# Kernel tuning notes

Measured on AMD Instinct MI355X. Metric: run time of the kernel, lower is better.

Reference implementation:

```python
import jax, jax.numpy as jnp
import numpy as np

Q_MAX = 127.0  # int8 symmetric quantization range

def _ste_round(v):
    # straight-through round (matches quantize-forward semantics)
    return v + jax.lax.stop_gradient(jnp.round(v) - v)

def setup_inputs() -> dict:
    key = jax.random.key(0)
    k1, k2, k3, k4 = jax.random.split(key, 4)
    B, S, D_IN, D_OUT = 32, 577, 1024, 2560
    x = jax.random.normal(k1, (B, S, D_IN), dtype=jnp.float32)
    # pre-quantized int8 weight stored as int32 for jax friendliness
    w_int = jax.random.randint(k2, (D_OUT, D_IN), -127, 128, dtype=jnp.int32)
    # per-output-row dequant scales (absmax/127 style, small positive)
    scale_w = jax.random.uniform(k3, (D_OUT,), dtype=jnp.float32, minval=0.005, maxval=0.02)
    bias = jax.random.normal(k4, (D_OUT,), dtype=jnp.float32)
    return {"x": x, "w_int": w_int, "scale_w": scale_w, "bias": bias}

def reference(x, w_int, scale_w, bias):
    # bnb Int8Linear: dynamic per-row int8 quantization of activations,
    # per-column (output-feature) weight scales, then bias add.
    # x: [B, S, D_in], w_int: [D_out, D_in] in [-127,127], scale_w: [D_out]
    absmax_x = jnp.max(jnp.abs(x), axis=-1, keepdims=True)  # [B, S, 1]
    scale_x = jnp.maximum(absmax_x, 1e-8) / Q_MAX
    x_q = _ste_round(x / scale_x)  # quantized activations in [-127, 127]
    # integer-valued GEMM carried in fp32 accumulation
    acc = jnp.einsum("bsd,od->bso", x_q, w_int.astype(jnp.float32))
    y = acc * scale_x * scale_w[None, None, :] + bias[None, None, :]
    return y
```

## Files before the change

### kernel.cpp

```cpp
#include <hip/hip_runtime.h>
#include <stdint.h>

typedef int v4i __attribute__((ext_vector_type(4)));

__device__ __forceinline__ void gll16(const void* g, void* l) {
    __builtin_amdgcn_global_load_lds(
        (const __attribute__((address_space(1))) void*)(uintptr_t)g,
        (__attribute__((address_space(3))) void*)(uint32_t)(uintptr_t)l,
        16, 0, 0);
}

__global__ __launch_bounds__(256) void quant_x(const float* __restrict__ x,
                                               signed char* __restrict__ xq,
                                               float* __restrict__ sx, int M) {
    const int row = blockIdx.x;
    const int tid = threadIdx.x;
    signed char* qrow = xq + (size_t)row * 1024;
    if (row >= M) {
        ((char4*)qrow)[tid] = make_char4(0, 0, 0, 0);
        if (tid == 0) sx[row] = 0.0f;
        return;
    }
    const float4 v = ((const float4*)(x + (size_t)row * 1024))[tid];
    float a = fmaxf(fmaxf(fabsf(v.x), fabsf(v.y)), fmaxf(fabsf(v.z), fabsf(v.w)));
#pragma unroll
    for (int off = 32; off > 0; off >>= 1)
        a = fmaxf(a, __shfl_xor(a, off));
    __shared__ float red[4];
    if ((tid & 63) == 0) red[tid >> 6] = a;
    __syncthreads();
    const float am = fmaxf(fmaxf(red[0], red[1]), fmaxf(red[2], red[3]));
    const float amc = fmaxf(am, 1e-8f);
    const float scale = amc * (1.0f / 127.0f);
    const float inv = 127.0f / amc;
    char4 q;
    q.x = (signed char)(int)rintf(v.x * inv);
    q.y = (signed char)(int)rintf(v.y * inv);
    q.z = (signed char)(int)rintf(v.z * inv);
    q.w = (signed char)(int)rintf(v.w * inv);
    ((char4*)qrow)[tid] = q;
    if (tid == 0) sx[row] = scale;
}

__global__ __launch_bounds__(256) void conv_w(const int* __restrict__ w,
                                              signed char* __restrict__ w8, int n4) {
    const int i = blockIdx.x * 256 + threadIdx.x;
    if (i < n4) {
        const int4 v = ((const int4*)w)[i];
        char4 c;
        c.x = (signed char)v.x; c.y = (signed char)v.y;
        c.z = (signed char)v.z; c.w = (signed char)v.w;
        ((char4*)w8)[i] = c;
    }
}

__global__ __launch_bounds__(256) void gemm_i8(const signed char* __restrict__ xq,
                                               const signed char* __restrict__ w8,
                                               const float* __restrict__ sx,
                                               const float* __restrict__ sw,
                                               const float* __restrict__ bias,
                                               float* __restrict__ out,
                                               int M, int N, int K) {
    __shared__ signed char As[128 * 64];
    __shared__ signed char Bs[128 * 64];

    const int tid  = threadIdx.x;
    const int lane = tid & 63;
    const int wave = tid >> 6;
    const int wm = (wave & 1) * 64;
    const int wn = (wave >> 1) * 64;
    const int m_block = blockIdx.y * 128;
    const int n_block = blockIdx.x * 128;

    v4i acc[4][4];
#pragma unroll
    for (int mt = 0; mt < 4; ++mt)
#pragma unroll
        for (int nt = 0; nt < 4; ++nt) {
            acc[mt][nt].x = 0; acc[mt][nt].y = 0; acc[mt][nt].z = 0; acc[mt][nt].w = 0;
        }

    const int sr = tid >> 2;
    const int sc = ((tid & 3) ^ ((sr >> 1) & 3)) * 16;
    const signed char* aG = xq + (size_t)(m_block + sr) * K + sc;
    const signed char* bG = w8 + (size_t)(n_block + sr) * K + sc;
    signed char* aL = As + wave * 1024;
    signed char* bL = Bs + wave * 1024;

    const int fr  = lane & 15;
    const int fcs = (((lane >> 4) ^ ((lane >> 1) & 3))) * 16;

    for (int k0 = 0; k0 < K; k0 += 64) {
        if (k0) __syncthreads();
        gll16(aG + k0, aL);
        gll16(aG + k0 + (size_t)64 * K, aL + 4096);
        gll16(bG + k0, bL);
        gll16(bG + k0 + (size_t)64 * K, bL + 4096);
        __syncthreads();

        v4i af[4], bf[4];
#pragma unroll
        for (int mt = 0; mt < 4; ++mt)
            af[mt] = *(const v4i*)&As[(wm + mt * 16 + fr) * 64 + fcs];
#pragma unroll
        for (int nt = 0; nt < 4; ++nt)
            bf[nt] = *(const v4i*)&Bs[(wn + nt * 16 + fr) * 64 + fcs];
#pragma unroll
        for (int mt = 0; mt < 4; ++mt)
#pragma unroll
            for (int nt = 0; nt < 4; ++nt)
                acc[mt][nt] = __builtin_amdgcn_mfma_i32_16x16x64_i8(af[mt], bf[nt], acc[mt][nt], 0, 0, 0);
    }

    const int lr = lane >> 4;
    const int lc = lane & 15;
#pragma unroll
    for (int mt = 0; mt < 4; ++mt) {
        const int rbase = m_block + wm + mt * 16 + lr * 4;
        float sxv[4];
#pragma unroll
        for (int r = 0; r < 4; ++r)
            sxv[r] = (rbase + r < M) ? sx[rbase + r] : 0.0f;
#pragma unroll
        for (int nt = 0; nt < 4; ++nt) {
            const int col = n_block + wn + nt * 16 + lc;
            const float swv = sw[col];
            const float bv  = bias[col];
            const int* a = (const int*)&acc[mt][nt];
#pragma unroll
            for (int r = 0; r < 4; ++r) {
                const int row = rbase + r;
                if (row < M)
                    out[(size_t)row * N + col] = (float)a[r] * sxv[r] * swv + bv;
            }
        }
    }
}

extern "C" void kernel_launch(void* const* d_in, const int* in_sizes, int n_in,
                              void* d_out, int out_size, void* d_ws, size_t ws_size,
                              hipStream_t stream) {
    const float* x       = (const float*)d_in[0];
    const int*   w_int   = (const int*)d_in[1];
    const float* scale_w = (const float*)d_in[2];
    const float* bias    = (const float*)d_in[3];
    float* out = (float*)d_out;

    const int D_OUT = in_sizes[2];
    const int D_IN  = in_sizes[1] / D_OUT;
    const int M     = in_sizes[0] / D_IN;
    const int Mpad  = ((M + 127) / 128) * 128;

    signed char* xq = (signed char*)d_ws;
    signed char* w8 = xq + (size_t)Mpad * D_IN;
    float*       sx = (float*)(w8 + (size_t)D_OUT * D_IN);

    quant_x<<<Mpad, 256, 0, stream>>>(x, xq, sx, M);
    const int n4 = D_OUT * D_IN / 4;
    conv_w<<<(n4 + 255) / 256, 256, 0, stream>>>(w_int, w8, n4);
    dim3 grid(D_OUT / 128, Mpad / 128);
    gemm_i8<<<grid, dim3(256, 1, 1), 0, stream>>>(xq, w8, sx, scale_w, bias, out, M, D_OUT, D_IN);
}
```

Before: 317.4 us.

## Enlarge GEMM tile to 256x256 with 8 waves and double-buffered LDS pipeline

The int8 GEMM moves from 128x128 tiles with 4 waves to 256x256 tiles with 8 waves, each wave computing 128x64. Shared memory is double-buffered with global-to-LDS prefetch two K-tiles ahead, manual vmcnt waits, and MFMA work split in two halves around the next stage issue, with raised wave priority during the MFMA sections. The goal is to hide global load latency and raise arithmetic intensity per LDS byte. The costs are more registers and LDS per block, fewer blocks in the grid, and more M padding.

Measured after the change: 324.5 us. 2.2% more time.

```diff
diff --git a/kernel.cpp b/kernel.cpp
--- a/kernel.cpp
+++ b/kernel.cpp
@@ -54,76 +54,104 @@
     }
 }
 
-__global__ __launch_bounds__(256) void gemm_i8(const signed char* __restrict__ xq,
-                                               const signed char* __restrict__ w8,
-                                               const float* __restrict__ sx,
-                                               const float* __restrict__ sw,
-                                               const float* __restrict__ bias,
-                                               float* __restrict__ out,
-                                               int M, int N, int K) {
-    __shared__ signed char As[128 * 64];
-    __shared__ signed char Bs[128 * 64];
+__global__ __launch_bounds__(512, 2) void gemm_i8(const signed char* __restrict__ xq,
+                                                  const signed char* __restrict__ w8,
+                                                  const float* __restrict__ sx,
+                                                  const float* __restrict__ sw,
+                                                  const float* __restrict__ bias,
+                                                  float* __restrict__ out,
+                                                  int M, int N, int K) {
+    __shared__ signed char As[2][16384];
+    __shared__ signed char Bs[2][16384];
 
     const int tid  = threadIdx.x;
     const int lane = tid & 63;
     const int wave = tid >> 6;
-    const int wm = (wave & 1) * 64;
-    const int wn = (wave >> 1) * 64;
-    const int m_block = blockIdx.y * 128;
-    const int n_block = blockIdx.x * 128;
+    const int m_off = (wave >> 2) * 128;
+    const int n_off = (wave & 3) * 64;
+    const int m_block = blockIdx.y * 256;
+    const int n_block = blockIdx.x * 256;
+    const int nt_tiles = K >> 6;
 
-    v4i acc[4][4];
+    v4i acc[8][4];
 #pragma unroll
-    for (int mt = 0; mt < 4; ++mt)
+    for (int mt = 0; mt < 8; ++mt)
 #pragma unroll
         for (int nt = 0; nt < 4; ++nt) {
             acc[mt][nt].x = 0; acc[mt][nt].y = 0; acc[mt][nt].z = 0; acc[mt][nt].w = 0;
         }
 
-    const int sr = tid >> 2;
-    const int sc = ((tid & 3) ^ ((sr >> 1) & 3)) * 16;
-    const signed char* aG = xq + (size_t)(m_block + sr) * K + sc;
-    const signed char* bG = w8 + (size_t)(n_block + sr) * K + sc;
-    signed char* aL = As + wave * 1024;
-    signed char* bL = Bs + wave * 1024;
+    const int sc = ((tid & 3) ^ ((tid >> 3) & 3)) * 16;
+    const signed char* sA = xq + (size_t)(m_block + (tid >> 2)) * K + sc;
+    const signed char* sB = w8 + (size_t)(n_block + (tid >> 2)) * K + sc;
 
-    const int fr  = lane & 15;
-    const int fcs = (((lane >> 4) ^ ((lane >> 1) & 3))) * 16;
+    auto stage = [&](int Tt, int bufi) {
+        const size_t ko = (size_t)Tt << 6;
+        gll16(sA + ko,                    &As[bufi][wave * 1024]);
+        gll16(sA + ko + ((size_t)K << 7), &As[bufi][wave * 1024 + 8192]);
+        gll16(sB + ko,                    &Bs[bufi][wave * 1024]);
+        gll16(sB + ko + ((size_t)K << 7), &Bs[bufi][wave * 1024 + 8192]);
+    };
 
-    for (int k0 = 0; k0 < K; k0 += 64) {
-        if (k0) __syncthreads();
-        gll16(aG + k0, aL);
-        gll16(aG + k0 + (size_t)64 * K, aL + 4096);
-        gll16(bG + k0, bL);
-        gll16(bG + k0 + (size_t)64 * K, bL + 4096);
-        __syncthreads();
+    const int fr = lane & 15;
+    const int off_frag = fr * 64 + (((lane >> 4) ^ ((fr >> 1) & 3)) * 16);
 
-        v4i af[4], bf[4];
+    stage(0, 0);
+    stage(1, 1);
+    asm volatile("s_waitcnt vmcnt(4)" ::: "memory");
+    __builtin_amdgcn_s_barrier();
+
+    for (int T = 0; T < nt_tiles; ++T) {
+        const int cur = T & 1;
+        v4i af[8], bf[4];
+        const signed char* Ab = &As[cur][m_off * 64 + off_frag];
+        const signed char* Bb = &Bs[cur][n_off * 64 + off_frag];
 #pragma unroll
-        for (int mt = 0; mt < 4; ++mt)
-            af[mt] = *(const v4i*)&As[(wm + mt * 16 + fr) * 64 + fcs];
+        for (int mt = 0; mt < 8; ++mt) af[mt] = *(const v4i*)(Ab + mt * 1024);
 #pragma unroll
-        for (int nt = 0; nt < 4; ++nt)
-            bf[nt] = *(const v4i*)&Bs[(wn + nt * 16 + fr) * 64 + fcs];
+        for (int nt = 0; nt < 4; ++nt) bf[nt] = *(const v4i*)(Bb + nt * 1024);
+
+        __builtin_amdgcn_s_barrier();
+        asm volatile("s_waitcnt lgkmcnt(0)" ::: "memory");
+        __builtin_amdgcn_s_setprio(1);
 #pragma unroll
         for (int mt = 0; mt < 4; ++mt)
 #pragma unroll
             for (int nt = 0; nt < 4; ++nt)
                 acc[mt][nt] = __builtin_amdgcn_mfma_i32_16x16x64_i8(af[mt], bf[nt], acc[mt][nt], 0, 0, 0);
+        __builtin_amdgcn_s_setprio(0);
+        __builtin_amdgcn_s_barrier();
+
+        if (T + 2 < nt_tiles) stage(T + 2, cur);
+
+        __builtin_amdgcn_s_setprio(1);
+#pragma unroll
+        for (int mt = 4; mt < 8; ++mt)
+#pragma unroll
+            for (int nt = 0; nt < 4; ++nt)
+                acc[mt][nt] = __builtin_amdgcn_mfma_i32_16x16x64_i8(af[mt], bf[nt], acc[mt][nt], 0, 0, 0);
+        __builtin_amdgcn_s_setprio(0);
+
+        if (T + 1 < nt_tiles) {
+            if (T + 2 < nt_tiles)
+                asm volatile("s_waitcnt vmcnt(4)" ::: "memory");
+            else
+                asm volatile("s_waitcnt vmcnt(0)" ::: "memory");
+            __builtin_amdgcn_s_barrier();
+        }
     }
 
     const int lr = lane >> 4;
     const int lc = lane & 15;
 #pragma unroll
-    for (int mt = 0; mt < 4; ++mt) {
-        const int rbase = m_block + wm + mt * 16 + lr * 4;
+    for (int mt = 0; mt < 8; ++mt) {
+        const int rbase = m_block + m_off + mt * 16 + lr * 4;
         float sxv[4];
 #pragma unroll
-        for (int r = 0; r < 4; ++r)
-            sxv[r] = (rbase + r < M) ? sx[rbase + r] : 0.0f;
+        for (int r = 0; r < 4; ++r) sxv[r] = sx[rbase + r];
 #pragma unroll
         for (int nt = 0; nt < 4; ++nt) {
-            const int col = n_block + wn + nt * 16 + lc;
+            const int col = n_block + n_off + nt * 16 + lc;
             const float swv = sw[col];
             const float bv  = bias[col];
             const int* a = (const int*)&acc[mt][nt];
@@ -149,7 +177,7 @@
     const int D_OUT = in_sizes[2];
     const int D_IN  = in_sizes[1] / D_OUT;
     const int M     = in_sizes[0] / D_IN;
-    const int Mpad  = ((M + 127) / 128) * 128;
+    const int Mpad  = ((M + 255) / 256) * 256;
 
     signed char* xq = (signed char*)d_ws;
     signed char* w8 = xq + (size_t)Mpad * D_IN;
@@ -158,6 +186,6 @@
     quant_x<<<Mpad, 256, 0, stream>>>(x, xq, sx, M);
     const int n4 = D_OUT * D_IN / 4;
     conv_w<<<(n4 + 255) / 256, 256, 0, stream>>>(w_int, w8, n4);
-    dim3 grid(D_OUT / 128, Mpad / 128);
-    gemm_i8<<<grid, dim3(256, 1, 1), 0, stream>>>(xq, w8, sx, scale_w, bias, out, M, D_OUT, D_IN);
+    dim3 grid(D_OUT / 256, Mpad / 256);
+    gemm_i8<<<grid, dim3(512, 1, 1), 0, stream>>>(xq, w8, sx, scale_w, bias, out, M, D_OUT, D_IN);
 }
```

## Double-buffer LDS tiles and switch to 32x32x32 int8 MFMA with register prefetch

Applied to the files above, without the earlier changes.

The GEMM gets double-buffered LDS, so tile T+2 is loaded asynchronously while tile T is computed, with explicit vmcnt waits and barriers. It swaps the 16x16x64 MFMAs for 32x32x32 int8 MFMAs and prefetches the next half-K fragments into registers. The aim is to hide global-load latency and cut the per-iteration full-barrier stalls. It also adds a launch_bounds occupancy hint of 3 blocks and doubles LDS usage to 32KB per block.

Result: no change. 315.1 us (-0.7%).

```diff
diff --git a/kernel.cpp b/kernel.cpp
--- a/kernel.cpp
+++ b/kernel.cpp
@@ -1,7 +1,8 @@
 #include <hip/hip_runtime.h>
 #include <stdint.h>
 
-typedef int v4i __attribute__((ext_vector_type(4)));
+typedef int v4i  __attribute__((ext_vector_type(4)));
+typedef int v16i __attribute__((ext_vector_type(16)));
 
 __device__ __forceinline__ void gll16(const void* g, void* l) {
     __builtin_amdgcn_global_load_lds(
@@ -54,87 +55,127 @@
     }
 }
 
-__global__ __launch_bounds__(256) void gemm_i8(const signed char* __restrict__ xq,
-                                               const signed char* __restrict__ w8,
-                                               const float* __restrict__ sx,
-                                               const float* __restrict__ sw,
-                                               const float* __restrict__ bias,
-                                               float* __restrict__ out,
-                                               int M, int N, int K) {
-    __shared__ signed char As[128 * 64];
-    __shared__ signed char Bs[128 * 64];
+__global__ __launch_bounds__(256, 3) void gemm_i8(const signed char* __restrict__ xq,
+                                                  const signed char* __restrict__ w8,
+                                                  const float* __restrict__ sx,
+                                                  const float* __restrict__ sw,
+                                                  const float* __restrict__ bias,
+                                                  float* __restrict__ out,
+                                                  int M, int N, int K) {
+    __shared__ signed char As[2][8192];
+    __shared__ signed char Bs[2][8192];
 
     const int tid  = threadIdx.x;
     const int lane = tid & 63;
     const int wave = tid >> 6;
-    const int wm = (wave & 1) * 64;
-    const int wn = (wave >> 1) * 64;
+    const int m_off = (wave >> 1) * 64;
+    const int n_off = (wave & 1) * 64;
     const int m_block = blockIdx.y * 128;
     const int n_block = blockIdx.x * 128;
-
-    v4i acc[4][4];
-#pragma unroll
-    for (int mt = 0; mt < 4; ++mt)
-#pragma unroll
-        for (int nt = 0; nt < 4; ++nt) {
-            acc[mt][nt].x = 0; acc[mt][nt].y = 0; acc[mt][nt].z = 0; acc[mt][nt].w = 0;
-        }
+    const int NT = K >> 6;
+
+    v16i acc[2][2];
+#pragma unroll
+    for (int mi = 0; mi < 2; ++mi)
+#pragma unroll
+        for (int ni = 0; ni < 2; ++ni)
+#pragma unroll
+            for (int e = 0; e < 16; ++e) acc[mi][ni][e] = 0;
 
     const int sr = tid >> 2;
     const int sc = ((tid & 3) ^ ((sr >> 1) & 3)) * 16;
     const signed char* aG = xq + (size_t)(m_block + sr) * K + sc;
     const signed char* bG = w8 + (size_t)(n_block + sr) * K + sc;
-    signed char* aL = As + wave * 1024;
-    signed char* bL = Bs + wave * 1024;
-
-    const int fr  = lane & 15;
-    const int fcs = (((lane >> 4) ^ ((lane >> 1) & 3))) * 16;
-
-    for (int k0 = 0; k0 < K; k0 += 64) {
-        if (k0) __syncthreads();
-        gll16(aG + k0, aL);
-        gll16(aG + k0 + (size_t)64 * K, aL + 4096);
-        gll16(bG + k0, bL);
-        gll16(bG + k0 + (size_t)64 * K, bL + 4096);
-        __syncthreads();
-
-        v4i af[4], bf[4];
-#pragma unroll
-        for (int mt = 0; mt < 4; ++mt)
-            af[mt] = *(const v4i*)&As[(wm + mt * 16 + fr) * 64 + fcs];
-#pragma unroll
-        for (int nt = 0; nt < 4; ++nt)
-            bf[nt] = *(const v4i*)&Bs[(wn + nt * 16 + fr) * 64 + fcs];
-#pragma unroll
-        for (int mt = 0; mt < 4; ++mt)
-#pragma unroll
-            for (int nt = 0; nt < 4; ++nt)
-                acc[mt][nt] = __builtin_amdgcn_mfma_i32_16x16x64_i8(af[mt], bf[nt], acc[mt][nt], 0, 0, 0);
+    const int ldst = wave * 1024;
+
+    auto stage = [&](int Tt, int b) {
+        const size_t ko = (size_t)Tt << 6;
+        gll16(aG + ko,                    &As[b][ldst]);
+        gll16(aG + ko + ((size_t)K << 6), &As[b][ldst + 4096]);
+        gll16(bG + ko,                    &Bs[b][ldst]);
+        gll16(bG + ko + ((size_t)K << 6), &Bs[b][ldst + 4096]);
+    };
+
+    const int rl  = lane & 31;
+    const int hi  = lane >> 5;
+    const int key = (rl >> 1) & 3;
+    const int ck0 = (hi ^ key) * 16;
+    const int ck1 = ((2 + hi) ^ key) * 16;
+    const int arow = (m_off + rl) * 64;
+    const int brow = (n_off + rl) * 64;
+
+    stage(0, 0);
+    stage(1, 1);
+    asm volatile("s_waitcnt vmcnt(4)" ::: "memory");
+    __builtin_amdgcn_s_barrier();
+
+    v4i a0, a1, b0, b1;
+    v4i na0, na1, nb0, nb1;
+    a0 = *(const v4i*)(As[0] + arow + ck0);
+    a1 = *(const v4i*)(As[0] + arow + 2048 + ck0);
+    b0 = *(const v4i*)(Bs[0] + brow + ck0);
+    b1 = *(const v4i*)(Bs[0] + brow + 2048 + ck0);
+
+    for (int T = 0; T < NT; ++T) {
+        const int cur = T & 1;
+        const signed char* Ac = As[cur];
+        const signed char* Bc = Bs[cur];
+        na0 = *(const v4i*)(Ac + arow + ck1);
+        na1 = *(const v4i*)(Ac + arow + 2048 + ck1);
+        nb0 = *(const v4i*)(Bc + brow + ck1);
+        nb1 = *(const v4i*)(Bc + brow + 2048 + ck1);
+
+        acc[0][0] = __builtin_amdgcn_mfma_i32_32x32x32_i8(a0, b0, acc[0][0], 0, 0, 0);
+        acc[0][1] = __builtin_amdgcn_mfma_i32_32x32x32_i8(a0, b1, acc[0][1], 0, 0, 0);
+        acc[1][0] = __builtin_amdgcn_mfma_i32_32x32x32_i8(a1, b0, acc[1][0], 0, 0, 0);
+        acc[1][1] = __builtin_amdgcn_mfma_i32_32x32x32_i8(a1, b1, acc[1][1], 0, 0, 0);
+
+        asm volatile("s_waitcnt lgkmcnt(0)" ::: "memory");
+        __builtin_amdgcn_s_barrier();
+
+        if (T + 2 < NT) stage(T + 2, cur);
+
+        if (T + 1 < NT) {
+            if (T + 2 < NT)
+                asm volatile("s_waitcnt vmcnt(4)" ::: "memory");
+            else
+                asm volatile("s_waitcnt vmcnt(0)" ::: "memory");
+            __builtin_amdgcn_s_barrier();
+            const signed char* An = As[cur ^ 1];
+            const signed char* Bn = Bs[cur ^ 1];
+            a0 = *(const v4i*)(An + arow + ck0);
+            a1 = *(const v4i*)(An + arow + 2048 + ck0);
+            b0 = *(const v4i*)(Bn + brow + ck0);
+            b1 = *(const v4i*)(Bn + brow + 2048 + ck0);
+        }
+
+        acc[0][0] = __builtin_amdgcn_mfma_i32_32x32x32_i8(na0, nb0, acc[0][0], 0, 0, 0);
+        acc[0][1] = __builtin_amdgcn_mfma_i32_32x32x32_i8(na0, nb1, acc[0][1], 0, 0, 0);
+        acc[1][0] = __builtin_amdgcn_mfma_i32_32x32x32_i8(na1, nb0, acc[1][0], 0, 0, 0);
+        acc[1][1] = __builtin_amdgcn_mfma_i32_32x32x32_i8(na1, nb1, acc[1][1], 0, 0, 0);
     }
 
-    const int lr = lane >> 4;
-    const int lc = lane & 15;
-#pragma unroll
-    for (int mt = 0; mt < 4; ++mt) {
-        const int rbase = m_block + wm + mt * 16 + lr * 4;
-        float sxv[4];
-#pragma unroll
-        for (int r = 0; r < 4; ++r)
-            sxv[r] = (rbase + r < M) ? sx[rbase + r] : 0.0f;
-#pragma unroll
-        for (int nt = 0; nt < 4; ++nt) {
-            const int col = n_block + wn + nt * 16 + lc;
-            const float swv = sw[col];
-            const float bv  = bias[col];
-            const int* a = (const int*)&acc[mt][nt];
-#pragma unroll
-            for (int r = 0; r < 4; ++r) {
-                const int row = rbase + r;
-                if (row < M)
-                    out[(size_t)row * N + col] = (float)a[r] * sxv[r] * swv + bv;
+#pragma unroll
+    for (int mi = 0; mi < 2; ++mi)
+#pragma unroll
+        for (int q = 0; q < 4; ++q) {
+            const int rbase = m_block + m_off + mi * 32 + q * 8 + hi * 4;
+            float sxv[4];
+#pragma unroll
+            for (int r = 0; r < 4; ++r) sxv[r] = sx[rbase + r];
+#pragma unroll
+            for (int ni = 0; ni < 2; ++ni) {
+                const int col = n_block + n_off + ni * 32 + rl;
+                const float swv = sw[col];
+                const float bv  = bias[col];
+#pragma unroll
+                for (int r = 0; r < 4; ++r) {
+                    const int row = rbase + r;
+                    if (row < M)
+                        out[(size_t)row * N + col] = (float)acc[mi][ni][q * 4 + r] * sxv[r] * swv + bv;
+                }
             }
         }
-    }
 }
 
 extern "C" void kernel_launch(void* const* d_in, const int* in_sizes, int n_in,
```
